# Kernel optimization log

Measured on AMD Instinct MI355X. Metric: run time of the kernel, lower is better.

The kernel has to match this reference:

```python
import jax, jax.numpy as jnp
import numpy as np

# Static CT geometry (ctlib-style): parallel-beam pixel-driven backprojection
VIEWS, DETS = 512, 512   # sinogram: angles x detector bins
H, W = 256, 256          # reconstructed image grid


def setup_inputs() -> dict:
    key = jax.random.key(0)
    proj = jax.random.normal(key, (4, 1, VIEWS, DETS), dtype=jnp.float32)
    # options = [dImg (pixel size), dDet (detector bin size), Ang0, dAng]
    options = jnp.array([1.0, 1.5, 0.0, np.pi / VIEWS], dtype=jnp.float32)
    return {"proj": proj, "options": options}


def reference(proj, options):
    # proj: [B, 1, VIEWS, DETS] sinogram; returns image [B, 1, H, W]
    dImg, dDet, ang0, dAng = options[0], options[1], options[2], options[3]

    ang = ang0 + dAng * jnp.arange(VIEWS, dtype=jnp.float32)          # [V]
    cos_a, sin_a = jnp.cos(ang), jnp.sin(ang)
    # pixel-center world coordinates (y axis points up)
    xs = (jnp.arange(W, dtype=jnp.float32) - (W - 1) / 2.0) * dImg     # [W]
    ys = ((H - 1) / 2.0 - jnp.arange(H, dtype=jnp.float32)) * dImg     # [H]

    # signed distance of each pixel to the detector axis for each view: t[v,y,x]
    t = cos_a[:, None, None] * xs[None, None, :] + sin_a[:, None, None] * ys[None, :, None]
    u = t / dDet + (DETS - 1) / 2.0                                    # fractional detector coord

    i0 = jnp.floor(u)
    w = u - i0                                                         # linear interp weight
    i0i = i0.astype(jnp.int32)
    i1i = i0i + 1
    m0 = ((i0i >= 0) & (i0i < DETS)).astype(proj.dtype)
    m1 = ((i1i >= 0) & (i1i < DETS)).astype(proj.dtype)
    i0c = jnp.clip(i0i, 0, DETS - 1)
    i1c = jnp.clip(i1i, 0, DETS - 1)

    p = proj[:, 0]                                                     # [B, V, D]
    vix = jnp.arange(VIEWS)[:, None, None]                             # [V,1,1]
    p0 = p[:, vix, i0c]                                                # [B, V, H, W]
    p1 = p[:, vix, i1c]
    val = p0 * ((1.0 - w) * m0) + p1 * (w * m1)                        # interpolated ray values

    img = dAng * jnp.sum(val, axis=1)                                  # accumulate over views
    return img[:, None, :, :]
```

## Files before the change

kernel.cpp:

```cpp
#include <hip/hip_runtime.h>
#include <math.h>

#define VIEWS  512
#define DETS   512
#define HH     256
#define WW     256
#define VSPLIT 8
#define VCHUNK (VIEWS / VSPLIT)
#define TS     32
#define CV     16
#define WIN    48
#define NCHUNK (VCHUNK / CV)

__global__ __launch_bounds__(256, 8) void backproj_kernel(
    const float* __restrict__ proj,
    const float* __restrict__ options,
    float* __restrict__ out)
{
    __shared__ float2 s_cs[VCHUNK];
    __shared__ float4 s_pk[2][CV];
    __shared__ float  s_win[2][CV][WIN];

    const float dImg = options[0];
    const float dDet = options[1];
    const float ang0 = options[2];
    const float dAng = options[3];

    const int tid = threadIdx.x;
    const int blk = blockIdx.x;
    const int vq  = blk & 7;
    const int tx  = (blk >> 3) & 7;
    const int ty  = (blk >> 6) & 7;
    const int b   = blk >> 9;
    const int v0  = vq * VCHUNK;
    const int x0t = tx * TS;
    const int y0t = ty * TS;

    if (tid < VCHUNK) {
        float a = ang0 + dAng * (float)(v0 + tid);
        float ss, cc;
        sincosf(a, &ss, &cc);
        s_cs[tid] = make_float2(cc, ss);
    }

    const float sc   = dImg / dDet;
    const float uoff = (DETS - 1) * 0.5f;

    const int xl = tid & 31;
    const int yg = tid >> 5;
    const float xs  = ((float)(x0t + xl) - (WW - 1) * 0.5f) * sc;
    const float ys0 = ((HH - 1) * 0.5f - (float)(y0t + yg * 4)) * sc;
    const float ys3 = ys0 - 3.0f * sc;

    const float xa = ((float)x0t - (WW - 1) * 0.5f) * sc;
    const float xb = ((float)(x0t + TS - 1) - (WW - 1) * 0.5f) * sc;
    const float ya = ((HH - 1) * 0.5f - (float)y0t) * sc;
    const float yb = ((HH - 1) * 0.5f - (float)(y0t + TS - 1)) * sc;

    const int sv = tid >> 4;
    const int sj = tid & 15;
    const float* __restrict__ pbase = proj + (size_t)(b * VIEWS + v0) * DETS;

    __syncthreads();

    float t0, t1, t2, cR, sR, w0f, dR;
    {
        float2 cs = s_cs[sv];
        cR = cs.x; sR = cs.y;
        float umin = fminf(cR * xa, cR * xb) + fminf(sR * ya, sR * yb) + uoff;
        w0f = floorf(umin) - 2.0f;
        dR  = sR * sc;
        const float* row = pbase + (size_t)sv * DETS + (int)w0f;
        t0 = row[sj]; t1 = row[sj + 16]; t2 = row[sj + 32];
    }
    s_win[0][sv][sj]      = t0;
    s_win[0][sv][sj + 16] = t1;
    s_win[0][sv][sj + 32] = t2;
    if (sj == 0) s_pk[0][sv] = make_float4(cR, sR, uoff - w0f, dR);
    __syncthreads();

    float acc0 = 0.f, acc1 = 0.f, acc2 = 0.f, acc3 = 0.f, accq = 0.f;

    for (int ch = 0; ch < NCHUNK; ++ch) {
        const int cur = ch & 1;
        const int nxt = cur ^ 1;

        if (ch + 1 < NCHUNK) {
            int gv = (ch + 1) * CV + sv;
            float2 cs = s_cs[gv];
            cR = cs.x; sR = cs.y;
            float umin = fminf(cR * xa, cR * xb) + fminf(sR * ya, sR * yb) + uoff;
            w0f = floorf(umin) - 2.0f;
            dR  = sR * sc;
            const float* row = pbase + (size_t)gv * DETS + (int)w0f;
            t0 = row[sj]; t1 = row[sj + 16]; t2 = row[sj + 32];
        }

#pragma unroll 4
        for (int vv = 0; vv < CV; ++vv) {
            float4 pk = s_pk[cur][vv];
            float tb  = fmaf(pk.x, xs, pk.z);
            float u0  = fmaf(pk.y, ys0, tb);
            float u3  = fmaf(pk.y, ys3, tb);
            float mF  = floorf(fminf(u0, u3));
            int   mi  = (int)mF;
            const float* win = s_win[cur][vv];
            float q0 = win[mi];
            float q1 = win[mi + 1];
            float q2 = win[mi + 2];
            float q3 = win[mi + 3];
            float d0 = q1 - q0, d1 = q2 - q1, d2 = q3 - q2;
            float f0 = u0 - mF;
            float f3 = u3 - mF;
            float dd = pk.w;
            float f1 = f0 - dd;
            float f2 = f3 + dd;
            accq += q0;
            {
                float c0 = fminf(f0, 1.0f);
                float c1 = fminf(fmaxf(f0 - 1.0f, 0.0f), 1.0f);
                float c2 = fminf(fmaxf(f0 - 2.0f, 0.0f), 1.0f);
                acc0 = fmaf(c0, d0, acc0); acc0 = fmaf(c1, d1, acc0); acc0 = fmaf(c2, d2, acc0);
            }
            {
                float c0 = fminf(f1, 1.0f);
                float c1 = fminf(fmaxf(f1 - 1.0f, 0.0f), 1.0f);
                float c2 = fminf(fmaxf(f1 - 2.0f, 0.0f), 1.0f);
                acc1 = fmaf(c0, d0, acc1); acc1 = fmaf(c1, d1, acc1); acc1 = fmaf(c2, d2, acc1);
            }
            {
                float c0 = fminf(f2, 1.0f);
                float c1 = fminf(fmaxf(f2 - 1.0f, 0.0f), 1.0f);
                float c2 = fminf(fmaxf(f2 - 2.0f, 0.0f), 1.0f);
                acc2 = fmaf(c0, d0, acc2); acc2 = fmaf(c1, d1, acc2); acc2 = fmaf(c2, d2, acc2);
            }
            {
                float c0 = fminf(f3, 1.0f);
                float c1 = fminf(fmaxf(f3 - 1.0f, 0.0f), 1.0f);
                float c2 = fminf(fmaxf(f3 - 2.0f, 0.0f), 1.0f);
                acc3 = fmaf(c0, d0, acc3); acc3 = fmaf(c1, d1, acc3); acc3 = fmaf(c2, d2, acc3);
            }
        }

        if (ch + 1 < NCHUNK) {
            s_win[nxt][sv][sj]      = t0;
            s_win[nxt][sv][sj + 16] = t1;
            s_win[nxt][sv][sj + 32] = t2;
            if (sj == 0) s_pk[nxt][sv] = make_float4(cR, sR, uoff - w0f, dR);
            __syncthreads();
        }
    }

    float* o = out + ((size_t)b * HH + (y0t + yg * 4)) * WW + x0t + xl;
    atomicAdd(o,                  (acc0 + accq) * dAng);
    atomicAdd(o + WW,             (acc1 + accq) * dAng);
    atomicAdd(o + 2 * (size_t)WW, (acc2 + accq) * dAng);
    atomicAdd(o + 3 * (size_t)WW, (acc3 + accq) * dAng);
}

extern "C" void kernel_launch(void* const* d_in, const int* in_sizes, int n_in,
                              void* d_out, int out_size, void* d_ws, size_t ws_size,
                              hipStream_t stream) {
    const float* proj    = (const float*)d_in[0];
    const float* options = (const float*)d_in[1];
    float* out = (float*)d_out;

    hipMemsetAsync(d_out, 0, (size_t)out_size * sizeof(float), stream);

    dim3 grid(4 * 64 * VSPLIT);
    dim3 block(256);
    backproj_kernel<<<grid, block, 0, stream>>>(proj, options, out);
}
```

Measured before the change: 87.71 us.

## Load whole view-chunk window into LDS once; precompute angle table in separate kernel

Replaces the double-buffered 16-view chunk pipeline with a single upfront load of all 64 views' detector windows into shared memory, with windows centered on the tile center instead of at the tile minimum. The sin/cos table moves to a tiny setup kernel that writes to workspace, and the per-view parameters are recomputed in the inner loop from global memory reads. This removes the per-chunk syncthreads and the in-loop staging. In exchange it raises LDS use to about 12KB per block, adds a kernel launch, and adds per-iteration global loads and extra arithmetic.

```diff
diff --git a/kernel.cpp b/kernel.cpp
--- a/kernel.cpp
+++ b/kernel.cpp
@@ -8,22 +8,28 @@
 #define VSPLIT 8
 #define VCHUNK (VIEWS / VSPLIT)
 #define TS     32
-#define CV     16
 #define WIN    48
-#define NCHUNK (VCHUNK / CV)
+
+__global__ void cs_setup(const float* __restrict__ options,
+                         float2* __restrict__ cst) {
+    int v = blockIdx.x * 256 + threadIdx.x;
+    if (v < VIEWS) {
+        float s, c;
+        sincosf(options[2] + options[3] * (float)v, &s, &c);
+        cst[v] = make_float2(c, s);
+    }
+}
 
 __global__ __launch_bounds__(256, 8) void backproj_kernel(
     const float* __restrict__ proj,
     const float* __restrict__ options,
+    const float2* __restrict__ cst,
     float* __restrict__ out)
 {
-    __shared__ float2 s_cs[VCHUNK];
-    __shared__ float4 s_pk[2][CV];
-    __shared__ float  s_win[2][CV][WIN];
+    __shared__ float s_win[VCHUNK][WIN];
 
     const float dImg = options[0];
     const float dDet = options[1];
-    const float ang0 = options[2];
     const float dAng = options[3];
 
     const int tid = threadIdx.x;
@@ -36,15 +42,11 @@
     const int x0t = tx * TS;
     const int y0t = ty * TS;
 
-    if (tid < VCHUNK) {
-        float a = ang0 + dAng * (float)(v0 + tid);
-        float ss, cc;
-        sincosf(a, &ss, &cc);
-        s_cs[tid] = make_float2(cc, ss);
-    }
-
     const float sc   = dImg / dDet;
     const float uoff = (DETS - 1) * 0.5f;
+
+    const float xcen = ((float)x0t + 15.5f - (WW - 1) * 0.5f) * sc;
+    const float ycen = ((HH - 1) * 0.5f - ((float)y0t + 15.5f)) * sc;
 
     const int xl = tid & 31;
     const int yg = tid >> 5;
@@ -52,102 +54,67 @@
     const float ys0 = ((HH - 1) * 0.5f - (float)(y0t + yg * 4)) * sc;
     const float ys3 = ys0 - 3.0f * sc;
 
-    const float xa = ((float)x0t - (WW - 1) * 0.5f) * sc;
-    const float xb = ((float)(x0t + TS - 1) - (WW - 1) * 0.5f) * sc;
-    const float ya = ((HH - 1) * 0.5f - (float)y0t) * sc;
-    const float yb = ((HH - 1) * 0.5f - (float)(y0t + TS - 1)) * sc;
-
-    const int sv = tid >> 4;
-    const int sj = tid & 15;
-    const float* __restrict__ pbase = proj + (size_t)(b * VIEWS + v0) * DETS;
-
-    __syncthreads();
-
-    float t0, t1, t2, cR, sR, w0f, dR;
     {
-        float2 cs = s_cs[sv];
-        cR = cs.x; sR = cs.y;
-        float umin = fminf(cR * xa, cR * xb) + fminf(sR * ya, sR * yb) + uoff;
-        w0f = floorf(umin) - 2.0f;
-        dR  = sR * sc;
-        const float* row = pbase + (size_t)sv * DETS + (int)w0f;
-        t0 = row[sj]; t1 = row[sj + 16]; t2 = row[sj + 32];
+        const int sv = tid >> 2;
+        const int sj = tid & 3;
+        float2 cs = cst[v0 + sv];
+        float uc  = fmaf(cs.x, xcen, fmaf(cs.y, ycen, uoff));
+        float w0f = floorf(uc) - 24.0f;
+        const float* row =
+            proj + ((size_t)(b * VIEWS + v0 + sv) * DETS) + (int)w0f;
+#pragma unroll
+        for (int k = 0; k < 12; ++k)
+            s_win[sv][sj + 4 * k] = row[sj + 4 * k];
     }
-    s_win[0][sv][sj]      = t0;
-    s_win[0][sv][sj + 16] = t1;
-    s_win[0][sv][sj + 32] = t2;
-    if (sj == 0) s_pk[0][sv] = make_float4(cR, sR, uoff - w0f, dR);
     __syncthreads();
 
     float acc0 = 0.f, acc1 = 0.f, acc2 = 0.f, acc3 = 0.f, accq = 0.f;
 
-    for (int ch = 0; ch < NCHUNK; ++ch) {
-        const int cur = ch & 1;
-        const int nxt = cur ^ 1;
-
-        if (ch + 1 < NCHUNK) {
-            int gv = (ch + 1) * CV + sv;
-            float2 cs = s_cs[gv];
-            cR = cs.x; sR = cs.y;
-            float umin = fminf(cR * xa, cR * xb) + fminf(sR * ya, sR * yb) + uoff;
-            w0f = floorf(umin) - 2.0f;
-            dR  = sR * sc;
-            const float* row = pbase + (size_t)gv * DETS + (int)w0f;
-            t0 = row[sj]; t1 = row[sj + 16]; t2 = row[sj + 32];
+#pragma unroll 4
+    for (int vv = 0; vv < VCHUNK; ++vv) {
+        float2 cs = cst[v0 + vv];
+        float uc  = fmaf(cs.x, xcen, fmaf(cs.y, ycen, uoff));
+        float w0f = floorf(uc) - 24.0f;
+        float tb  = fmaf(cs.x, xs, uoff - w0f);
+        float u0  = fmaf(cs.y, ys0, tb);
+        float u3  = fmaf(cs.y, ys3, tb);
+        float mF  = floorf(fminf(u0, u3));
+        int   mi  = (int)mF;
+        const float* win = s_win[vv];
+        float q0 = win[mi];
+        float q1 = win[mi + 1];
+        float q2 = win[mi + 2];
+        float q3 = win[mi + 3];
+        float d0 = q1 - q0, d1 = q2 - q1, d2 = q3 - q2;
+        float dd = cs.y * sc;
+        float f0 = u0 - mF;
+        float f3 = u3 - mF;
+        float f1 = f0 - dd;
+        float f2 = f3 + dd;
+        accq += q0;
+        {
+            float c0 = fminf(f0, 1.0f);
+            float c1 = fminf(fmaxf(f0 - 1.0f, 0.0f), 1.0f);
+            float c2 = fminf(fmaxf(f0 - 2.0f, 0.0f), 1.0f);
+            acc0 = fmaf(c0, d0, acc0); acc0 = fmaf(c1, d1, acc0); acc0 = fmaf(c2, d2, acc0);
         }
-
-#pragma unroll 4
-        for (int vv = 0; vv < CV; ++vv) {
-            float4 pk = s_pk[cur][vv];
-            float tb  = fmaf(pk.x, xs, pk.z);
-            float u0  = fmaf(pk.y, ys0, tb);
-            float u3  = fmaf(pk.y, ys3, tb);
-            float mF  = floorf(fminf(u0, u3));
-            int   mi  = (int)mF;
-            const float* win = s_win[cur][vv];
-            float q0 = win[mi];
-            float q1 = win[mi + 1];
-            float q2 = win[mi + 2];
-            float q3 = win[mi + 3];
-            float d0 = q1 - q0, d1 = q2 - q1, d2 = q3 - q2;
-            float f0 = u0 - mF;
-            float f3 = u3 - mF;
-            float dd = pk.w;
-            float f1 = f0 - dd;
-            float f2 = f3 + dd;
-            accq += q0;
-            {
-                float c0 = fminf(f0, 1.0f);
-                float c1 = fminf(fmaxf(f0 - 1.0f, 0.0f), 1.0f);
-                float c2 = fminf(fmaxf(f0 - 2.0f, 0.0f), 1.0f);
-                acc0 = fmaf(c0, d0, acc0); acc0 = fmaf(c1, d1, acc0); acc0 = fmaf(c2, d2, acc0);
-            }
-            {
-                float c0 = fminf(f1, 1.0f);
-                float c1 = fminf(fmaxf(f1 - 1.0f, 0.0f), 1.0f);
-                float c2 = fminf(fmaxf(f1 - 2.0f, 0.0f), 1.0f);
-                acc1 = fmaf(c0, d0, acc1); acc1 = fmaf(c1, d1, acc1); acc1 = fmaf(c2, d2, acc1);
-            }
-            {
-                float c0 = fminf(f2, 1.0f);
-                float c1 = fminf(fmaxf(f2 - 1.0f, 0.0f), 1.0f);
-                float c2 = fminf(fmaxf(f2 - 2.0f, 0.0f), 1.0f);
-                acc2 = fmaf(c0, d0, acc2); acc2 = fmaf(c1, d1, acc2); acc2 = fmaf(c2, d2, acc2);
-            }
-            {
-                float c0 = fminf(f3, 1.0f);
-                float c1 = fminf(fmaxf(f3 - 1.0f, 0.0f), 1.0f);
-                float c2 = fminf(fmaxf(f3 - 2.0f, 0.0f), 1.0f);
-                acc3 = fmaf(c0, d0, acc3); acc3 = fmaf(c1, d1, acc3); acc3 = fmaf(c2, d2, acc3);
-            }
+        {
+            float c0 = fminf(f1, 1.0f);
+            float c1 = fminf(fmaxf(f1 - 1.0f, 0.0f), 1.0f);
+            float c2 = fminf(fmaxf(f1 - 2.0f, 0.0f), 1.0f);
+            acc1 = fmaf(c0, d0, acc1); acc1 = fmaf(c1, d1, acc1); acc1 = fmaf(c2, d2, acc1);
         }
-
-        if (ch + 1 < NCHUNK) {
-            s_win[nxt][sv][sj]      = t0;
-            s_win[nxt][sv][sj + 16] = t1;
-            s_win[nxt][sv][sj + 32] = t2;
-            if (sj == 0) s_pk[nxt][sv] = make_float4(cR, sR, uoff - w0f, dR);
-            __syncthreads();
+        {
+            float c0 = fminf(f2, 1.0f);
+            float c1 = fminf(fmaxf(f2 - 1.0f, 0.0f), 1.0f);
+            float c2 = fminf(fmaxf(f2 - 2.0f, 0.0f), 1.0f);
+            acc2 = fmaf(c0, d0, acc2); acc2 = fmaf(c1, d1, acc2); acc2 = fmaf(c2, d2, acc2);
+        }
+        {
+            float c0 = fminf(f3, 1.0f);
+            float c1 = fminf(fmaxf(f3 - 1.0f, 0.0f), 1.0f);
+            float c2 = fminf(fmaxf(f3 - 2.0f, 0.0f), 1.0f);
+            acc3 = fmaf(c0, d0, acc3); acc3 = fmaf(c1, d1, acc3); acc3 = fmaf(c2, d2, acc3);
         }
     }
 
@@ -163,11 +130,14 @@
                               hipStream_t stream) {
     const float* proj    = (const float*)d_in[0];
     const float* options = (const float*)d_in[1];
-    float* out = (float*)d_out;
+    float* out  = (float*)d_out;
+    float2* cst = (float2*)d_ws;
 
     hipMemsetAsync(d_out, 0, (size_t)out_size * sizeof(float), stream);
 
+    cs_setup<<<dim3(2), dim3(256), 0, stream>>>(options, cst);
+
     dim3 grid(4 * 64 * VSPLIT);
     dim3 block(256);
-    backproj_kernel<<<grid, block, 0, stream>>>(proj, options, out);
+    backproj_kernel<<<grid, block, 0, stream>>>(proj, options, cst, out);
 }
```

After: 88.11 us. No clear change (+0.5%).
